# Performance work log

Hardware: AMD Instinct MI355X
Metric: run time of the kernel (lower is better)

The kernel has to match this reference:

```python
import jax, jax.numpy as jnp
import numpy as np

L, H, E, CUTOFF = 3, 128, 20, 5.0
N_NODES, N_EDGES = 10000, 160000
NUM_EMBED = 119


def _linear(key, fin, fout):
    kw, kb = jax.random.split(key)
    s = 1.0 / np.sqrt(fin)
    W = jax.random.uniform(kw, (fin, fout), minval=-s, maxval=s, dtype=jnp.float32)
    b = jax.random.uniform(kb, (fout,), minval=-s, maxval=s, dtype=jnp.float32)
    return W, b


def _stack(key, fin, fout):
    Ws, bs = zip(*[_linear(k, fin, fout) for k in jax.random.split(key, L)])
    return jnp.stack(Ws), jnp.stack(bs)


def setup_inputs() -> dict:
    key = jax.random.key(0)
    ks = jax.random.split(key, 14)
    z = jax.random.randint(ks[0], (N_NODES,), 0, NUM_EMBED)
    edge = jax.random.randint(ks[1], (N_EDGES, 2), 0, N_NODES)
    edge_diff = jax.random.normal(ks[2], (N_EDGES, 3), dtype=jnp.float32) * 1.5
    edge_dist = jnp.linalg.norm(edge_diff, axis=-1) + 1e-2  # consistent unit vectors, strictly > 0
    embed = jax.random.normal(ks[3], (NUM_EMBED, H), dtype=jnp.float32)
    msg_filter_w, msg_filter_b = _stack(ks[4], E, 3 * H)
    msg_w1, msg_b1 = _stack(ks[5], H, H)
    msg_w2, msg_b2 = _stack(ks[6], H, 3 * H)
    upd_U_w, upd_U_b = _stack(ks[7], H, H)
    upd_V_w, upd_V_b = _stack(ks[8], H, H)
    upd_w1, upd_b1 = _stack(ks[9], 2 * H, H)
    upd_w2, upd_b2 = _stack(ks[10], H, 3 * H)
    ro_w1, ro_b1 = _linear(ks[11], H, H)
    ro_w2, ro_b2 = _linear(ks[12], H, H)
    return dict(z=z, edge=edge, edge_diff=edge_diff, edge_dist=edge_dist, embed=embed,
                msg_filter_w=msg_filter_w, msg_filter_b=msg_filter_b,
                msg_w1=msg_w1, msg_b1=msg_b1, msg_w2=msg_w2, msg_b2=msg_b2,
                upd_U_w=upd_U_w, upd_U_b=upd_U_b, upd_V_w=upd_V_w, upd_V_b=upd_V_b,
                upd_w1=upd_w1, upd_b1=upd_b1, upd_w2=upd_w2, upd_b2=upd_b2,
                ro_w1=ro_w1, ro_b1=ro_b1, ro_w2=ro_w2, ro_b2=ro_b2)


def _silu(x):
    return x * jax.nn.sigmoid(x)


def reference(z, edge, edge_diff, edge_dist, embed,
              msg_filter_w, msg_filter_b, msg_w1, msg_b1, msg_w2, msg_b2,
              upd_U_w, upd_U_b, upd_V_w, upd_V_b, upd_w1, upd_b1, upd_w2, upd_b2,
              ro_w1, ro_b1, ro_w2, ro_b2):
    N = z.shape[0]
    pi = jnp.asarray(np.pi, dtype=edge_dist.dtype)
    # sinc radial basis: sin(n*pi*d/cutoff)/d, n=1..E  -> [E_edges, E]
    n = jnp.arange(1, E + 1, dtype=edge_dist.dtype)
    rbf = jnp.sin(edge_dist[:, None] * n * pi / CUTOFF) / edge_dist[:, None]
    # cosine cutoff [E_edges]
    fcut = jnp.where(edge_dist < CUTOFF, 0.5 * (jnp.cos(pi * edge_dist / CUTOFF) + 1.0), 0.0)
    unit = edge_diff / edge_dist[:, None]  # [E_edges, 3]
    src = edge[:, 1]
    dst = edge[:, 0]

    node_scalar = embed[z]                                       # [N, H]
    node_vector = jnp.zeros((N, 3, H), dtype=edge_diff.dtype)    # [N, 3, H]

    for l in range(L):
        # --- message ---
        filter_w = (rbf @ msg_filter_w[l] + msg_filter_b[l]) * fcut[:, None]   # [E_edges, 3H]
        scalar_out = _silu(node_scalar @ msg_w1[l] + msg_b1[l]) @ msg_w2[l] + msg_b2[l]  # [N, 3H]
        filter_out = filter_w * scalar_out[src]                                 # gather + mul
        gate_sv, gate_ev, msg_s = jnp.split(filter_out, 3, axis=1)
        msg_v = node_vector[src] * gate_sv[:, None, :] + gate_ev[:, None, :] * unit[:, :, None]
        node_scalar = node_scalar + jax.ops.segment_sum(msg_s, dst, num_segments=N)
        node_vector = node_vector + jax.ops.segment_sum(msg_v, dst, num_segments=N)
        # --- update ---
        Uv = node_vector @ upd_U_w[l] + upd_U_b[l]   # [N, 3, H]
        Vv = node_vector @ upd_V_w[l] + upd_V_b[l]
        Vv_norm = jnp.linalg.norm(Vv, axis=1)        # [N, H]
        mlp_in = jnp.concatenate((Vv_norm, node_scalar), axis=1)
        mlp_out = _silu(mlp_in @ upd_w1[l] + upd_b1[l]) @ upd_w2[l] + upd_b2[l]
        a_vv, a_sv, a_ss = jnp.split(mlp_out, 3, axis=1)
        node_vector = node_vector + a_vv[:, None, :] * Uv
        node_scalar = node_scalar + a_sv * jnp.sum(Uv * Vv, axis=1) + a_ss

    # readout MLP
    return _silu(node_scalar @ ro_w1 + ro_b1) @ ro_w2 + ro_b2
```

## Files before the change

kernel.cpp:

```cpp
#include <hip/hip_runtime.h>
#include <hip/hip_bf16.h>

typedef __hip_bfloat16 bf16;
typedef __attribute__((ext_vector_type(8))) short bf16x8;
typedef __attribute__((ext_vector_type(4))) float f32x4;

#define H 128
#define F3H 384
#define E_RBF 20
#define NLAYER 3

__device__ __forceinline__ float silu_f(float x) { return x / (1.0f + __expf(-x)); }
__device__ __forceinline__ float b2f(bf16 x) { return __bfloat162float(x); }

constexpr float PI_F = 3.14159265358979323846f;
constexpr float CUT = 5.0f;

__global__ __launch_bounds__(256) void csr_hist(
    const int* __restrict__ edge, int* __restrict__ cnt, int nE) {
  int e = blockIdx.x * blockDim.x + threadIdx.x;
  if (e < nE) atomicAdd(&cnt[edge[2 * e]], 1);
}

__global__ __launch_bounds__(1024) void csr_scan(
    const int* __restrict__ cnt, int* __restrict__ rowstart, int* __restrict__ cur, int N) {
  __shared__ int part[1024];
  int t = threadIdx.x;
  int chunk = (N + 1023) / 1024;
  int lo = t * chunk; if (lo > N) lo = N;
  int hi = lo + chunk; if (hi > N) hi = N;
  int s = 0;
  for (int i = lo; i < hi; i++) s += cnt[i];
  part[t] = s;
  __syncthreads();
  for (int off = 1; off < 1024; off <<= 1) {
    int v = (t >= off) ? part[t - off] : 0;
    __syncthreads();
    part[t] += v;
    __syncthreads();
  }
  int r = (t == 0) ? 0 : part[t - 1];
  for (int i = lo; i < hi; i++) { rowstart[i] = r; cur[i] = r; r += cnt[i]; }
}

__global__ __launch_bounds__(256) void csr_fill_pack(
    const int* __restrict__ edge, int* __restrict__ cur,
    const float* __restrict__ edist, const float* __restrict__ ediff,
    int* __restrict__ srcs, float* __restrict__ geo, int nE) {
  int e = blockIdx.x * blockDim.x + threadIdx.x;
  if (e >= nE) return;
  int d = edge[2 * e];
  int p = atomicAdd(&cur[d], 1);
  srcs[p] = edge[2 * e + 1];
  float dd = edist[e];
  float inv = 1.0f / dd;
  float th = dd * (PI_F / CUT);
  float s1 = sinf(th), c1 = cosf(th);
  float fc = (dd < CUT) ? 0.5f * (c1 + 1.0f) : 0.0f;
  float* g = geo + (size_t)p * 24;
  float twoc = 2.0f * c1;
  float skp = 0.0f, sk = s1;
  #pragma unroll
  for (int k = 0; k < E_RBF; k++) {
    g[k] = sk * inv * fc;
    float nx = twoc * sk - skp;
    skp = sk; sk = nx;
  }
  g[20] = ediff[3 * (size_t)e] * inv;
  g[21] = ediff[3 * (size_t)e + 1] * inv;
  g[22] = ediff[3 * (size_t)e + 2] * inv;
  g[23] = fc;
}

__device__ __forceinline__ void pack_w_item(
    const float* __restrict__ Wu, const float* __restrict__ Wv,
    bf16* __restrict__ wp, int t) {
  int lane = t & 63;
  int c    = (t >> 6) & 7;
  int kb   = (t >> 9) & 3;
  int mat  = (t >> 11) & 1;
  int l    = t >> 12;
  const float* src = (mat ? Wv : Wu) + (size_t)l * H * H;
  bf16* dst = wp + ((size_t)(l * 2 + mat) * 16384) + (((kb * 8 + c) * 64 + lane) * 8);
  int quad = lane >> 4;
  int n = c * 16 + (lane & 15);
  #pragma unroll
  for (int j = 0; j < 8; j++) {
    int k = kb * 32 + quad * 8 + j;
    dst[j] = __float2bfloat16(src[(size_t)k * H + n]);
  }
}

__device__ __forceinline__ void pack_b_item(
    const float* __restrict__ src, bf16* __restrict__ dst,
    int K, int ncols, int t) {
  int kblocks = K >> 5, ncols16 = ncols >> 4;
  int lane = t & 63;
  int idx = t >> 6;
  int c = idx % ncols16; idx /= ncols16;
  int kb = idx % kblocks; idx /= kblocks;
  int l = idx;
  const float* s = src + (size_t)l * K * ncols;
  bf16* d = dst + (size_t)l * K * ncols + (((kb * ncols16 + c) * 64 + lane) * 8);
  int quad = lane >> 4;
  int n = c * 16 + (lane & 15);
  #pragma unroll
  for (int j = 0; j < 8; j++) {
    int k = kb * 32 + quad * 8 + j;
    d[j] = __float2bfloat16(s[(size_t)k * ncols + n]);
  }
}

__global__ __launch_bounds__(256) void pack_all(
    const float* __restrict__ Wu, const float* __restrict__ Wv, bf16* __restrict__ wpack,
    const float* __restrict__ uw1, bf16* __restrict__ wp_m1,
    const float* __restrict__ uw2, bf16* __restrict__ wp_m2,
    const float* __restrict__ mw1, bf16* __restrict__ wp_sm1,
    const float* __restrict__ mw2, bf16* __restrict__ wp_sm2,
    const float* __restrict__ rw1, bf16* __restrict__ wp_ro1,
    const float* __restrict__ rw2, bf16* __restrict__ wp_ro2,
    const int* __restrict__ z, const float* __restrict__ embed,
    float* __restrict__ ns, bf16* __restrict__ ns16,
    int* __restrict__ cnt, int N) {
  const int T0 = 12288;
  const int T1 = T0 + 12288;
  const int T2 = T1 + 18432;
  const int T3 = T2 + 6144;
  const int T4 = T3 + 18432;
  const int T5 = T4 + 2048;
  const int T6 = T5 + 2048;
  const int TN = T6 + N * H;
  const int TT = TN + N;
  for (int t = blockIdx.x * blockDim.x + threadIdx.x; t < TT; t += gridDim.x * blockDim.x) {
    if (t < T0)      pack_w_item(Wu, Wv, wpack, t);
    else if (t < T1) pack_b_item(uw1, wp_m1, 256, 128, t - T0);
    else if (t < T2) pack_b_item(uw2, wp_m2, 128, 384, t - T1);
    else if (t < T3) pack_b_item(mw1, wp_sm1, 128, 128, t - T2);
    else if (t < T4) pack_b_item(mw2, wp_sm2, 128, 384, t - T3);
    else if (t < T5) pack_b_item(rw1, wp_ro1, 128, 128, t - T4);
    else if (t < T6) pack_b_item(rw2, wp_ro2, 128, 128, t - T5);
    else if (t < TN) {
      int u = t - T6;
      int i = u >> 7, h = u & 127;
      float v = embed[(size_t)z[i] * H + h];
      ns[(size_t)i * H + h] = v;
      ns16[(size_t)i * H + h] = __float2bfloat16(v);
    } else {
      cnt[t - TN] = 0;
    }
  }
}

__global__ __launch_bounds__(256) void mlp_msg(
    const bf16* __restrict__ A, const bf16* __restrict__ Wp1,
    const float* __restrict__ b1, const bf16* __restrict__ Wp2,
    const float* __restrict__ b2, bf16* __restrict__ so, int M) {
  __shared__ bf16 m1l[32][136];
  int wave = threadIdx.x >> 6, lane = threadIdx.x & 63;
  int rowg = wave >> 1, ch = wave & 1;
  int r0 = blockIdx.x * 32 + rowg * 16;
  int quad = lane >> 4, nn = lane & 15;
  int arow = r0 + nn; if (arow >= M) arow = M - 1;
  f32x4 acc[4] = {};
  for (int kb = 0; kb < 4; kb++) {
    bf16x8 af = *(const bf16x8*)&A[(size_t)arow * H + kb * 32 + quad * 8];
    #pragma unroll
    for (int c = 0; c < 4; c++) {
      int cg = ch * 4 + c;
      bf16x8 bw = *(const bf16x8*)&Wp1[(((kb * 8 + cg) * 64) + lane) * 8];
      acc[c] = __builtin_amdgcn_mfma_f32_16x16x32_bf16(af, bw, acc[c], 0, 0, 0);
    }
  }
  #pragma unroll
  for (int c = 0; c < 4; c++) {
    int n = (ch * 4 + c) * 16 + nn;
    float bb = b1[n];
    #pragma unroll
    for (int r = 0; r < 4; r++) {
      int lr = rowg * 16 + quad * 4 + r;
      m1l[lr][n] = __float2bfloat16(silu_f(acc[c][r] + bb));
    }
  }
  __syncthreads();
  f32x4 a0[4] = {}, a1[4] = {}, a2[4] = {};
  for (int kb = 0; kb < 4; kb++) {
    bf16x8 af = *(const bf16x8*)&m1l[rowg * 16 + nn][kb * 32 + quad * 8];
    #pragma unroll
    for (int c = 0; c < 4; c++) {
      int cg = ch * 4 + c;
      bf16x8 b0 = *(const bf16x8*)&Wp2[(((kb * 24 + cg) * 64) + lane) * 8];
      bf16x8 b1v = *(const bf16x8*)&Wp2[(((kb * 24 + cg + 8) * 64) + lane) * 8];
      bf16x8 b2v = *(const bf16x8*)&Wp2[(((kb * 24 + cg + 16) * 64) + lane) * 8];
      a0[c] = __builtin_amdgcn_mfma_f32_16x16x32_bf16(af, b0, a0[c], 0, 0, 0);
      a1[c] = __builtin_amdgcn_mfma_f32_16x16x32_bf16(af, b1v, a1[c], 0, 0, 0);
      a2[c] = __builtin_amdgcn_mfma_f32_16x16x32_bf16(af, b2v, a2[c], 0, 0, 0);
    }
  }
  #pragma unroll
  for (int c = 0; c < 4; c++) {
    int n = (ch * 4 + c) * 16 + nn;
    float bb0 = b2[n], bb1 = b2[H + n], bb2 = b2[2 * H + n];
    #pragma unroll
    for (int r = 0; r < 4; r++) {
      int row = r0 + quad * 4 + r;
      if (row < M) {
        so[(size_t)row * F3H + n]           = __float2bfloat16(a0[c][r] + bb0);
        so[(size_t)row * F3H + H + n]       = __float2bfloat16(a1[c][r] + bb1);
        so[(size_t)row * F3H + 2 * H + n]   = __float2bfloat16(a2[c][r] + bb2);
      }
    }
  }
}

__global__ __launch_bounds__(384, 3) void uv_upd(
    const bf16* __restrict__ A, const bf16* __restrict__ Wpuv,
    const float* __restrict__ bu, const float* __restrict__ bv,
    const bf16* __restrict__ nsmsg,
    const bf16* __restrict__ Wp1, const float* __restrict__ b1,
    const bf16* __restrict__ Wp2, const float* __restrict__ b2,
    float* __restrict__ ns, bf16* __restrict__ ns16,
    float* __restrict__ nv, bf16* __restrict__ nvb16, int N) {
  __shared__ float Uv_l[48][132];
  __shared__ float Vv_l[48][132];
  __shared__ bf16 vn_l[16][136];
  __shared__ bf16 m1l[16][136];
  int wave = threadIdx.x >> 6;
  int lane = threadIdx.x & 63;
  int quad = lane >> 4, nn = lane & 15;
  int M3 = 3 * N;

  {
    int wt = (wave >= 3) ? wave - 3 : wave;
    bool isV = wave >= 3;
    int r0 = blockIdx.x * 48 + wt * 16;
    int arow = r0 + nn; if (arow >= M3) arow = M3 - 1;
    const bf16* Wb = Wpuv + (isV ? 16384 : 0);
    f32x4 acc[8] = {};
    for (int kb = 0; kb < 4; kb++) {
      bf16x8 af = *(const bf16x8*)&A[(size_t)arow * H + kb * 32 + quad * 8];
      #pragma unroll
      for (int c = 0; c < 8; c++) {
        bf16x8 bw = *(const bf16x8*)&Wb[(((kb * 8 + c) * 64) + lane) * 8];
        acc[c] = __builtin_amdgcn_mfma_f32_16x16x32_bf16(af, bw, acc[c], 0, 0, 0);
      }
    }
    const float* bias = isV ? bv : bu;
    #pragma unroll
    for (int c = 0; c < 8; c++) {
      int n = c * 16 + nn;
      float bb = bias[n];
      #pragma unroll
      for (int r = 0; r < 4; r++) {
        int lr = wt * 16 + quad * 4 + r;
        if (isV) Vv_l[lr][n] = acc[c][r] + bb;
        else     Uv_l[lr][n] = acc[c][r] + bb;
      }
    }
  }
  __syncthreads();

  for (int t = threadIdx.x; t < 16 * H; t += 384) {
    int node = t >> 7, hh = t & 127;
    float v0 = Vv_l[node * 3][hh];
    float v1 = Vv_l[node * 3 + 1][hh];
    float v2 = Vv_l[node * 3 + 2][hh];
    vn_l[node][hh] = __float2bfloat16(sqrtf(v0 * v0 + v1 * v1 + v2 * v2));
  }
  __syncthreads();

  int r0n = blockIdx.x * 16;
  int arown = r0n + nn; if (arown >= N) arown = N - 1;
  for (int g = wave; g < 8; g += 6) {
    f32x4 acc = {};
    for (int kb = 0; kb < 8; kb++) {
      bf16x8 af;
      if (kb < 4) af = *(const bf16x8*)&vn_l[nn][kb * 32 + quad * 8];
      else        af = *(const bf16x8*)&nsmsg[(size_t)arown * H + (kb - 4) * 32 + quad * 8];
      bf16x8 bw = *(const bf16x8*)&Wp1[(((kb * 8 + g) * 64) + lane) * 8];
      acc = __builtin_amdgcn_mfma_f32_16x16x32_bf16(af, bw, acc, 0, 0, 0);
    }
    int n = g * 16 + nn;
    float bb = b1[n];
    #pragma unroll
    for (int r = 0; r < 4; r++) {
      m1l[quad * 4 + r][n] = __float2bfloat16(silu_f(acc[r] + bb));
    }
  }
  __syncthreads();

  for (int g = wave; g < 8; g += 6) {
    f32x4 aav = {}, aas = {}, asz = {};
    for (int kb = 0; kb < 4; kb++) {
      bf16x8 af = *(const bf16x8*)&m1l[nn][kb * 32 + quad * 8];
      bf16x8 b0 = *(const bf16x8*)&Wp2[(((kb * 24 + g) * 64) + lane) * 8];
      bf16x8 b1v = *(const bf16x8*)&Wp2[(((kb * 24 + g + 8) * 64) + lane) * 8];
      bf16x8 b2v = *(const bf16x8*)&Wp2[(((kb * 24 + g + 16) * 64) + lane) * 8];
      aav = __builtin_amdgcn_mfma_f32_16x16x32_bf16(af, b0, aav, 0, 0, 0);
      aas = __builtin_amdgcn_mfma_f32_16x16x32_bf16(af, b1v, aas, 0, 0, 0);
      asz = __builtin_amdgcn_mfma_f32_16x16x32_bf16(af, b2v, asz, 0, 0, 0);
    }
    int n = g * 16 + nn;
    float bav = b2[n], bas = b2[H + n], bss = b2[2 * H + n];
    #pragma unroll
    for (int r = 0; r < 4; r++) {
      int row = r0n + quad * 4 + r;
      if (row < N) {
        int lrn = quad * 4 + r;
        float avv = aav[r] + bav;
        float asv = aas[r] + bas;
        float ass = asz[r] + bss;
        float u0 = Uv_l[lrn * 3 + 0][n];
        float u1 = Uv_l[lrn * 3 + 1][n];
        float u2 = Uv_l[lrn * 3 + 2][n];
        float v0 = Vv_l[lrn * 3 + 0][n];
        float v1 = Vv_l[lrn * 3 + 1][n];
        float v2 = Vv_l[lrn * 3 + 2][n];
        float dot = u0 * v0 + u1 * v1 + u2 * v2;
        float ns_new = ns[(size_t)row * H + n] + asv * dot + ass;
        ns[(size_t)row * H + n] = ns_new;
        ns16[(size_t)row * H + n] = __float2bfloat16(ns_new);
        float n0 = nv[(size_t)(3 * row + 0) * H + n] + avv * u0;
        float n1 = nv[(size_t)(3 * row + 1) * H + n] + avv * u1;
        float n2 = nv[(size_t)(3 * row + 2) * H + n] + avv * u2;
        nv[(size_t)(3 * row + 0) * H + n] = n0;
        nv[(size_t)(3 * row + 1) * H + n] = n1;
        nv[(size_t)(3 * row + 2) * H + n] = n2;
        nvb16[(size_t)(3 * row + 0) * H + n] = __float2bfloat16(n0);
        nvb16[(size_t)(3 * row + 1) * H + n] = __float2bfloat16(n1);
        nvb16[(size_t)(3 * row + 2) * H + n] = __float2bfloat16(n2);
      }
    }
  }
}

__global__ __launch_bounds__(256) void mlp_ro(
    const bf16* __restrict__ A, const bf16* __restrict__ Wp1,
    const float* __restrict__ b1, const bf16* __restrict__ Wp2,
    const float* __restrict__ b2, float* __restrict__ out, int M) {
  __shared__ bf16 m1l[32][136];
  int wave = threadIdx.x >> 6, lane = threadIdx.x & 63;
  int rowg = wave >> 1, ch = wave & 1;
  int r0 = blockIdx.x * 32 + rowg * 16;
  int quad = lane >> 4, nn = lane & 15;
  int arow = r0 + nn; if (arow >= M) arow = M - 1;
  f32x4 acc[4] = {};
  for (int kb = 0; kb < 4; kb++) {
    bf16x8 af = *(const bf16x8*)&A[(size_t)arow * H + kb * 32 + quad * 8];
    #pragma unroll
    for (int c = 0; c < 4; c++) {
      int cg = ch * 4 + c;
      bf16x8 bw = *(const bf16x8*)&Wp1[(((kb * 8 + cg) * 64) + lane) * 8];
      acc[c] = __builtin_amdgcn_mfma_f32_16x16x32_bf16(af, bw, acc[c], 0, 0, 0);
    }
  }
  #pragma unroll
  for (int c = 0; c < 4; c++) {
    int n = (ch * 4 + c) * 16 + nn;
    float bb = b1[n];
    #pragma unroll
    for (int r = 0; r < 4; r++) {
      int lr = rowg * 16 + quad * 4 + r;
      m1l[lr][n] = __float2bfloat16(silu_f(acc[c][r] + bb));
    }
  }
  __syncthreads();
  f32x4 a2[4] = {};
  for (int kb = 0; kb < 4; kb++) {
    bf16x8 af = *(const bf16x8*)&m1l[rowg * 16 + nn][kb * 32 + quad * 8];
    #pragma unroll
    for (int c = 0; c < 4; c++) {
      int cg = ch * 4 + c;
      bf16x8 bw = *(const bf16x8*)&Wp2[(((kb * 8 + cg) * 64) + lane) * 8];
      a2[c] = __builtin_amdgcn_mfma_f32_16x16x32_bf16(af, bw, a2[c], 0, 0, 0);
    }
  }
  #pragma unroll
  for (int c = 0; c < 4; c++) {
    int n = (ch * 4 + c) * 16 + nn;
    float bb = b2[n];
    #pragma unroll
    for (int r = 0; r < 4; r++) {
      int row = r0 + quad * 4 + r;
      if (row < M) out[(size_t)row * H + n] = a2[c][r] + bb;
    }
  }
}

template<bool HASNV>
__global__ __launch_bounds__(128, 4) void message3(
    const int* __restrict__ srcs, const int* __restrict__ rowstart,
    const int* __restrict__ cnt, const float* __restrict__ geo,
    const float* __restrict__ Wf, const float* __restrict__ bfb,
    const bf16* __restrict__ so, const bf16* __restrict__ nvb16,
    const float* __restrict__ nvA,
    float* __restrict__ ns, float* __restrict__ nvB,
    bf16* __restrict__ nvmsg16, bf16* __restrict__ nsmsg, int N) {
  int i = blockIdx.x;
  int h = threadIdx.x;

  float wf0[E_RBF], wf1[E_RBF], wf2[E_RBF];
  #pragma unroll
  for (int k = 0; k < E_RBF; k++) {
    wf0[k] = Wf[k * F3H + h];
    wf1[k] = Wf[k * F3H + H + h];
    wf2[k] = Wf[k * F3H + 2 * H + h];
  }
  float bb0 = bfb[h], bb1 = bfb[H + h], bb2 = bfb[2 * H + h];

  float accs = 0.0f, a0 = 0.0f, a1 = 0.0f, a2 = 0.0f;
  int jlo = rowstart[i], jhi = jlo + cnt[i];
  int j = jlo;
  for (; j + 1 < jhi; j += 2) {
    int s0 = srcs[j];
    int s1 = srcs[j + 1];
    const bf16* sop0 = so + (size_t)s0 * F3H;
    const bf16* sop1 = so + (size_t)s1 * F3H;
    float sA0 = b2f(sop0[h]), sB0 = b2f(sop0[H + h]), sC0 = b2f(sop0[2 * H + h]);
    float sA1 = b2f(sop1[h]), sB1 = b2f(sop1[H + h]), sC1 = b2f(sop1[2 * H + h]);
    float nA0, nB0, nC0, nA1, nB1, nC1;
    if (HASNV) {
      const bf16* nvp0 = nvb16 + (size_t)s0 * F3H;
      const bf16* nvp1 = nvb16 + (size_t)s1 * F3H;
      nA0 = b2f(nvp0[h]); nB0 = b2f(nvp0[H + h]); nC0 = b2f(nvp0[2 * H + h]);
      nA1 = b2f(nvp1[h]); nB1 = b2f(nvp1[H + h]); nC1 = b2f(nvp1[2 * H + h]);
    }

    {
      const float* g = geo + (size_t)j * 24;
      float gg[24];
      #pragma unroll
      for (int q = 0; q < 6; q++) *(float4*)&gg[4 * q] = *(const float4*)&g[4 * q];
      float fc = gg[23];
      float f0 = bb0 * fc, f1 = bb1 * fc, f2 = bb2 * fc;
      #pragma unroll
      for (int k = 0; k < E_RBF; k++) {
        float rk = gg[k];
        f0 += rk * wf0[k];
        f1 += rk * wf1[k];
        f2 += rk * wf2[k];
      }
      float u0 = gg[20], u1 = gg[21], u2 = gg[22];
      float gsv = f0 * sA0;
      float gev = f1 * sB0;
      accs += f2 * sC0;
      if (HASNV) {
        a0 += nA0 * gsv + gev * u0;
        a1 += nB0 * gsv + gev * u1;
        a2 += nC0 * gsv + gev * u2;
      } else {
        a0 += gev * u0;
        a1 += gev * u1;
        a2 += gev * u2;
      }
    }
    {
      const float* g = geo + (size_t)(j + 1) * 24;
      float gg[24];
      #pragma unroll
      for (int q = 0; q < 6; q++) *(float4*)&gg[4 * q] = *(const float4*)&g[4 * q];
      float fc = gg[23];
      float f0 = bb0 * fc, f1 = bb1 * fc, f2 = bb2 * fc;
      #pragma unroll
      for (int k = 0; k < E_RBF; k++) {
        float rk = gg[k];
        f0 += rk * wf0[k];
        f1 += rk * wf1[k];
        f2 += rk * wf2[k];
      }
      float u0 = gg[20], u1 = gg[21], u2 = gg[22];
      float gsv = f0 * sA1;
      float gev = f1 * sB1;
      accs += f2 * sC1;
      if (HASNV) {
        a0 += nA1 * gsv + gev * u0;
        a1 += nB1 * gsv + gev * u1;
        a2 += nC1 * gsv + gev * u2;
      } else {
        a0 += gev * u0;
        a1 += gev * u1;
        a2 += gev * u2;
      }
    }
  }
  if (j < jhi) {
    int src = srcs[j];
    const float* g = geo + (size_t)j * 24;
    float gg[24];
    #pragma unroll
    for (int q = 0; q < 6; q++) *(float4*)&gg[4 * q] = *(const float4*)&g[4 * q];
    float fc = gg[23];
    float f0 = bb0 * fc, f1 = bb1 * fc, f2 = bb2 * fc;
    #pragma unroll
    for (int k = 0; k < E_RBF; k++) {
      float rk = gg[k];
      f0 += rk * wf0[k];
      f1 += rk * wf1[k];
      f2 += rk * wf2[k];
    }
    float u0 = gg[20], u1 = gg[21], u2 = gg[22];
    const bf16* sop = so + (size_t)src * F3H;
    float gsv = f0 * b2f(sop[h]);
    float gev = f1 * b2f(sop[H + h]);
    accs += f2 * b2f(sop[2 * H + h]);
    if (HASNV) {
      const bf16* nvp = nvb16 + (size_t)src * F3H;
      a0 += b2f(nvp[h])         * gsv + gev * u0;
      a1 += b2f(nvp[H + h])     * gsv + gev * u1;
      a2 += b2f(nvp[2 * H + h]) * gsv + gev * u2;
    } else {
      a0 += gev * u0;
      a1 += gev * u1;
      a2 += gev * u2;
    }
  }

  float ns_new = ns[(size_t)i * H + h] + accs;
  ns[(size_t)i * H + h] = ns_new;
  nsmsg[(size_t)i * H + h] = __float2bfloat16(ns_new);
  float o0, o1, o2;
  if (HASNV) {
    const float* nvi = nvA + (size_t)i * F3H;
    o0 = nvi[h] + a0;
    o1 = nvi[H + h] + a1;
    o2 = nvi[2 * H + h] + a2;
  } else {
    o0 = a0; o1 = a1; o2 = a2;
  }
  nvB[(size_t)i * F3H + h]         = o0;
  nvB[(size_t)i * F3H + H + h]     = o1;
  nvB[(size_t)i * F3H + 2 * H + h] = o2;
  nvmsg16[(size_t)i * F3H + h]         = __float2bfloat16(o0);
  nvmsg16[(size_t)i * F3H + H + h]     = __float2bfloat16(o1);
  nvmsg16[(size_t)i * F3H + 2 * H + h] = __float2bfloat16(o2);
}

extern "C" void kernel_launch(void* const* d_in, const int* in_sizes, int n_in,
                              void* d_out, int out_size, void* d_ws, size_t ws_size,
                              hipStream_t stream) {
  const int*   z     = (const int*)d_in[0];
  const int*   edge  = (const int*)d_in[1];
  const float* ediff = (const float*)d_in[2];
  const float* edist = (const float*)d_in[3];
  const float* embed = (const float*)d_in[4];
  const float* mfw   = (const float*)d_in[5];
  const float* mfb   = (const float*)d_in[6];
  const float* mw1   = (const float*)d_in[7];
  const float* mb1   = (const float*)d_in[8];
  const float* mw2   = (const float*)d_in[9];
  const float* mb2   = (const float*)d_in[10];
  const float* uUw   = (const float*)d_in[11];
  const float* uUb   = (const float*)d_in[12];
  const float* uVw   = (const float*)d_in[13];
  const float* uVb   = (const float*)d_in[14];
  const float* uw1   = (const float*)d_in[15];
  const float* ub1   = (const float*)d_in[16];
  const float* uw2   = (const float*)d_in[17];
  const float* ub2   = (const float*)d_in[18];
  const float* rw1   = (const float*)d_in[19];
  const float* rb1   = (const float*)d_in[20];
  const float* rw2   = (const float*)d_in[21];
  const float* rb2   = (const float*)d_in[22];

  const int N  = in_sizes[0];
  const int nE = in_sizes[3];

  float* ws = (float*)d_ws;
  size_t off = 0;
  float* ns      = ws + off; off += (size_t)N * H;
  float* nvA     = ws + off; off += (size_t)N * F3H;
  float* nvB     = ws + off; off += (size_t)N * F3H;
  float* geo     = ws + off; off += (size_t)nE * 24;
  bf16* so       = (bf16*)(ws + off); off += (size_t)N * F3H / 2;
  bf16* nvb16    = (bf16*)(ws + off); off += (size_t)N * F3H / 2;
  bf16* nvmsg16  = (bf16*)(ws + off); off += (size_t)N * F3H / 2;
  bf16* nsmsg    = (bf16*)(ws + off); off += (size_t)N * 64;
  bf16* ns16     = (bf16*)(ws + off); off += (size_t)N * 64;
  bf16* wpack    = (bf16*)(ws + off); off += 3 * 2 * 16384 / 2;
  bf16* wp_m1    = (bf16*)(ws + off); off += 3 * 256 * 128 / 2;
  bf16* wp_m2    = (bf16*)(ws + off); off += 3 * 128 * 384 / 2;
  bf16* wp_sm1   = (bf16*)(ws + off); off += 3 * 128 * 128 / 2;
  bf16* wp_sm2   = (bf16*)(ws + off); off += 3 * 128 * 384 / 2;
  bf16* wp_ro1   = (bf16*)(ws + off); off += 128 * 128 / 2;
  bf16* wp_ro2   = (bf16*)(ws + off); off += 128 * 128 / 2;
  int* srcs     = (int*)(ws + off); off += nE;
  int* cnt      = (int*)(ws + off); off += N;
  int* rowstart = (int*)(ws + off); off += N;
  int* cur      = (int*)(ws + off); off += N;

  const int tilesN = (N + 31) / 32;
  const int tilesUV = (N + 15) / 16;

  pack_all<<<1024, 256, 0, stream>>>(
      uUw, uVw, wpack, uw1, wp_m1, uw2, wp_m2, mw1, wp_sm1, mw2, wp_sm2,
      rw1, wp_ro1, rw2, wp_ro2, z, embed, ns, ns16, cnt, N);
  csr_hist<<<(nE + 255) / 256, 256, 0, stream>>>(edge, cnt, nE);
  csr_scan<<<1, 1024, 0, stream>>>(cnt, rowstart, cur, N);
  csr_fill_pack<<<(nE + 255) / 256, 256, 0, stream>>>(edge, cur, edist, ediff, srcs, geo, nE);

  float* nv_cur = nvA;
  float* nv_nxt = nvB;
  for (int l = 0; l < NLAYER; l++) {
    mlp_msg<<<tilesN, 256, 0, stream>>>(
        ns16, wp_sm1 + (size_t)l * 128 * 128, mb1 + (size_t)l * H,
        wp_sm2 + (size_t)l * 128 * 384, mb2 + (size_t)l * F3H, so, N);

    if (l == 0)
      message3<false><<<N, H, 0, stream>>>(srcs, rowstart, cnt, geo,
                                           mfw + (size_t)l * E_RBF * F3H, mfb + (size_t)l * F3H,
                                           so, nvb16, nv_cur, ns, nv_nxt, nvmsg16, nsmsg, N);
    else
      message3<true><<<N, H, 0, stream>>>(srcs, rowstart, cnt, geo,
                                          mfw + (size_t)l * E_RBF * F3H, mfb + (size_t)l * F3H,
                                          so, nvb16, nv_cur, ns, nv_nxt, nvmsg16, nsmsg, N);

    uv_upd<<<tilesUV, 384, 0, stream>>>(
        nvmsg16, wpack + (size_t)l * 2 * 16384,
        uUb + (size_t)l * H, uVb + (size_t)l * H,
        nsmsg,
        wp_m1 + (size_t)l * 256 * 128, ub1 + (size_t)l * H,
        wp_m2 + (size_t)l * 128 * 384, ub2 + (size_t)l * F3H,
        ns, ns16, nv_nxt, nvb16, N);

    float* t = nv_cur; nv_cur = nv_nxt; nv_nxt = t;
  }

  mlp_ro<<<tilesN, 256, 0, stream>>>(
      ns16, wp_ro1, rb1, wp_ro2, rb2, (float*)d_out, N);
}
```

Measured before the change: 453.8 us.

## Fuse next-layer message MLP and readout MLP into update kernel epilogue

```diff
diff --git a/kernel.cpp b/kernel.cpp
--- a/kernel.cpp
+++ b/kernel.cpp
@@ -212,14 +212,18 @@
   }
 }
 
+template<int MODE>
 __global__ __launch_bounds__(384, 3) void uv_upd(
     const bf16* __restrict__ A, const bf16* __restrict__ Wpuv,
     const float* __restrict__ bu, const float* __restrict__ bv,
     const bf16* __restrict__ nsmsg,
     const bf16* __restrict__ Wp1, const float* __restrict__ b1,
     const bf16* __restrict__ Wp2, const float* __restrict__ b2,
-    float* __restrict__ ns, bf16* __restrict__ ns16,
-    float* __restrict__ nv, bf16* __restrict__ nvb16, int N) {
+    float* __restrict__ ns,
+    float* __restrict__ nv, bf16* __restrict__ nvb16,
+    const bf16* __restrict__ Wx1, const float* __restrict__ bx1,
+    const bf16* __restrict__ Wx2, const float* __restrict__ bx2,
+    bf16* __restrict__ so, float* __restrict__ out, int N) {
   __shared__ float Uv_l[48][132];
   __shared__ float Vv_l[48][132];
   __shared__ bf16 vn_l[16][136];
@@ -318,7 +322,7 @@
         float dot = u0 * v0 + u1 * v1 + u2 * v2;
         float ns_new = ns[(size_t)row * H + n] + asv * dot + ass;
         ns[(size_t)row * H + n] = ns_new;
-        ns16[(size_t)row * H + n] = __float2bfloat16(ns_new);
+        vn_l[lrn][n] = __float2bfloat16(ns_new);
         float n0 = nv[(size_t)(3 * row + 0) * H + n] + avv * u0;
         float n1 = nv[(size_t)(3 * row + 1) * H + n] + avv * u1;
         float n2 = nv[(size_t)(3 * row + 2) * H + n] + avv * u2;
@@ -331,57 +335,63 @@
       }
     }
   }
-}
-
-__global__ __launch_bounds__(256) void mlp_ro(
-    const bf16* __restrict__ A, const bf16* __restrict__ Wp1,
-    const float* __restrict__ b1, const bf16* __restrict__ Wp2,
-    const float* __restrict__ b2, float* __restrict__ out, int M) {
-  __shared__ bf16 m1l[32][136];
-  int wave = threadIdx.x >> 6, lane = threadIdx.x & 63;
-  int rowg = wave >> 1, ch = wave & 1;
-  int r0 = blockIdx.x * 32 + rowg * 16;
-  int quad = lane >> 4, nn = lane & 15;
-  int arow = r0 + nn; if (arow >= M) arow = M - 1;
-  f32x4 acc[4] = {};
-  for (int kb = 0; kb < 4; kb++) {
-    bf16x8 af = *(const bf16x8*)&A[(size_t)arow * H + kb * 32 + quad * 8];
-    #pragma unroll
-    for (int c = 0; c < 4; c++) {
-      int cg = ch * 4 + c;
-      bf16x8 bw = *(const bf16x8*)&Wp1[(((kb * 8 + cg) * 64) + lane) * 8];
-      acc[c] = __builtin_amdgcn_mfma_f32_16x16x32_bf16(af, bw, acc[c], 0, 0, 0);
-    }
-  }
-  #pragma unroll
-  for (int c = 0; c < 4; c++) {
-    int n = (ch * 4 + c) * 16 + nn;
-    float bb = b1[n];
+  __syncthreads();
+
+  for (int g = wave; g < 8; g += 6) {
+    f32x4 acc = {};
+    for (int kb = 0; kb < 4; kb++) {
+      bf16x8 af = *(const bf16x8*)&vn_l[nn][kb * 32 + quad * 8];
+      bf16x8 bw = *(const bf16x8*)&Wx1[(((kb * 8 + g) * 64) + lane) * 8];
+      acc = __builtin_amdgcn_mfma_f32_16x16x32_bf16(af, bw, acc, 0, 0, 0);
+    }
+    int n = g * 16 + nn;
+    float bb = bx1[n];
     #pragma unroll
     for (int r = 0; r < 4; r++) {
-      int lr = rowg * 16 + quad * 4 + r;
-      m1l[lr][n] = __float2bfloat16(silu_f(acc[c][r] + bb));
+      m1l[quad * 4 + r][n] = __float2bfloat16(silu_f(acc[r] + bb));
     }
   }
   __syncthreads();
-  f32x4 a2[4] = {};
-  for (int kb = 0; kb < 4; kb++) {
-    bf16x8 af = *(const bf16x8*)&m1l[rowg * 16 + nn][kb * 32 + quad * 8];
-    #pragma unroll
-    for (int c = 0; c < 4; c++) {
-      int cg = ch * 4 + c;
-      bf16x8 bw = *(const bf16x8*)&Wp2[(((kb * 8 + cg) * 64) + lane) * 8];
-      a2[c] = __builtin_amdgcn_mfma_f32_16x16x32_bf16(af, bw, a2[c], 0, 0, 0);
-    }
-  }
-  #pragma unroll
-  for (int c = 0; c < 4; c++) {
-    int n = (ch * 4 + c) * 16 + nn;
-    float bb = b2[n];
-    #pragma unroll
-    for (int r = 0; r < 4; r++) {
-      int row = r0 + quad * 4 + r;
-      if (row < M) out[(size_t)row * H + n] = a2[c][r] + bb;
+
+  if (MODE == 0) {
+    for (int g = wave; g < 8; g += 6) {
+      f32x4 a0 = {}, a1 = {}, a2 = {};
+      for (int kb = 0; kb < 4; kb++) {
+        bf16x8 af = *(const bf16x8*)&m1l[nn][kb * 32 + quad * 8];
+        bf16x8 b0 = *(const bf16x8*)&Wx2[(((kb * 24 + g) * 64) + lane) * 8];
+        bf16x8 b1v = *(const bf16x8*)&Wx2[(((kb * 24 + g + 8) * 64) + lane) * 8];
+        bf16x8 b2v = *(const bf16x8*)&Wx2[(((kb * 24 + g + 16) * 64) + lane) * 8];
+        a0 = __builtin_amdgcn_mfma_f32_16x16x32_bf16(af, b0, a0, 0, 0, 0);
+        a1 = __builtin_amdgcn_mfma_f32_16x16x32_bf16(af, b1v, a1, 0, 0, 0);
+        a2 = __builtin_amdgcn_mfma_f32_16x16x32_bf16(af, b2v, a2, 0, 0, 0);
+      }
+      int n = g * 16 + nn;
+      float bb0 = bx2[n], bb1 = bx2[H + n], bb2 = bx2[2 * H + n];
+      #pragma unroll
+      for (int r = 0; r < 4; r++) {
+        int row = r0n + quad * 4 + r;
+        if (row < N) {
+          so[(size_t)row * F3H + n]         = __float2bfloat16(a0[r] + bb0);
+          so[(size_t)row * F3H + H + n]     = __float2bfloat16(a1[r] + bb1);
+          so[(size_t)row * F3H + 2 * H + n] = __float2bfloat16(a2[r] + bb2);
+        }
+      }
+    }
+  } else {
+    for (int g = wave; g < 8; g += 6) {
+      f32x4 acc = {};
+      for (int kb = 0; kb < 4; kb++) {
+        bf16x8 af = *(const bf16x8*)&m1l[nn][kb * 32 + quad * 8];
+        bf16x8 bw = *(const bf16x8*)&Wx2[(((kb * 8 + g) * 64) + lane) * 8];
+        acc = __builtin_amdgcn_mfma_f32_16x16x32_bf16(af, bw, acc, 0, 0, 0);
+      }
+      int n = g * 16 + nn;
+      float bb = bx2[n];
+      #pragma unroll
+      for (int r = 0; r < 4; r++) {
+        int row = r0n + quad * 4 + r;
+        if (row < N) out[(size_t)row * H + n] = acc[r] + bb;
+      }
     }
   }
 }
@@ -600,9 +610,9 @@
   float* nv_cur = nvA;
   float* nv_nxt = nvB;
   for (int l = 0; l < NLAYER; l++) {
-    mlp_msg<<<tilesN, 256, 0, stream>>>(
-        ns16, wp_sm1 + (size_t)l * 128 * 128, mb1 + (size_t)l * H,
-        wp_sm2 + (size_t)l * 128 * 384, mb2 + (size_t)l * F3H, so, N);
+    if (l == 0)
+      mlp_msg<<<tilesN, 256, 0, stream>>>(
+          ns16, wp_sm1, mb1, wp_sm2, mb2, so, N);
 
     if (l == 0)
       message3<false><<<N, H, 0, stream>>>(srcs, rowstart, cnt, geo,
@@ -613,17 +623,29 @@
                                           mfw + (size_t)l * E_RBF * F3H, mfb + (size_t)l * F3H,
                                           so, nvb16, nv_cur, ns, nv_nxt, nvmsg16, nsmsg, N);
 
-    uv_upd<<<tilesUV, 384, 0, stream>>>(
-        nvmsg16, wpack + (size_t)l * 2 * 16384,
-        uUb + (size_t)l * H, uVb + (size_t)l * H,
-        nsmsg,
-        wp_m1 + (size_t)l * 256 * 128, ub1 + (size_t)l * H,
-        wp_m2 + (size_t)l * 128 * 384, ub2 + (size_t)l * F3H,
-        ns, ns16, nv_nxt, nvb16, N);
+    if (l < NLAYER - 1) {
+      uv_upd<0><<<tilesUV, 384, 0, stream>>>(
+          nvmsg16, wpack + (size_t)l * 2 * 16384,
+          uUb + (size_t)l * H, uVb + (size_t)l * H,
+          nsmsg,
+          wp_m1 + (size_t)l * 256 * 128, ub1 + (size_t)l * H,
+          wp_m2 + (size_t)l * 128 * 384, ub2 + (size_t)l * F3H,
+          ns, nv_nxt, nvb16,
+          wp_sm1 + (size_t)(l + 1) * 128 * 128, mb1 + (size_t)(l + 1) * H,
+          wp_sm2 + (size_t)(l + 1) * 128 * 384, mb2 + (size_t)(l + 1) * F3H,
+          so, nullptr, N);
+    } else {
+      uv_upd<1><<<tilesUV, 384, 0, stream>>>(
+          nvmsg16, wpack + (size_t)l * 2 * 16384,
+          uUb + (size_t)l * H, uVb + (size_t)l * H,
+          nsmsg,
+          wp_m1 + (size_t)l * 256 * 128, ub1 + (size_t)l * H,
+          wp_m2 + (size_t)l * 128 * 384, ub2 + (size_t)l * F3H,
+          ns, nv_nxt, nvb16,
+          wp_ro1, rb1, wp_ro2, rb2,
+          nullptr, (float*)d_out, N);
+    }
 
     float* t = nv_cur; nv_cur = nv_nxt; nv_nxt = t;
   }
-
-  mlp_ro<<<tilesN, 256, 0, stream>>>(
-      ns16, wp_ro1, rb1, wp_ro2, rb2, (float*)d_out, N);
-}
+}
```

After: 461.1 us. No clear change (+1.6%).
